# Kernel optimization log

Measured on AMD Instinct MI355X. Metric: run time of the kernel, lower is better.

Reference implementation:

```python
import jax, jax.numpy as jnp
import numpy as np

B, T, HID = 2, 2048, 1024
NH = 8
QK_DIM = 1024
V_DIM = 2048
SCALE_BASE = 512.0
GN_EPS = 1e-5


def _xpos_rotate(x, downscale):
    # x: [B, T, QK_DIM]; XPOS rotary embedding (syncdoth/RetNet, offset=0)
    d = QK_DIM
    dh = d // 2
    pos = jnp.arange(T, dtype=jnp.float32)
    # per-pair magnitude scale
    base_scale = (jnp.arange(0, d, 2, dtype=jnp.float32) + 0.4 * d) / (1.4 * d)  # [dh]
    scale = base_scale[None, :] ** (pos[:, None] / SCALE_BASE)  # [T, dh]
    if downscale:
        scale = 1.0 / scale
    inv_freq = 1.0 / (10000.0 ** (jnp.arange(dh, dtype=jnp.float32) / dh))
    sinusoid = pos[:, None] * inv_freq[None, :]  # [T, dh]
    sin = jnp.sin(sinusoid) * scale
    cos = jnp.cos(sinusoid) * scale
    # duplicate_interleave -> [T, d]
    sin = jnp.repeat(sin, 2, axis=-1)
    cos = jnp.repeat(cos, 2, axis=-1)
    x1 = x[..., 0::2]
    x2 = x[..., 1::2]
    rot = jnp.stack((-x2, x1), axis=-1).reshape(x.shape)  # rotate_every_two
    return x * cos[None] + rot * sin[None]


def setup_inputs() -> dict:
    key = jax.random.key(0)
    k1, k2, k3, k4 = jax.random.split(key, 4)
    x = jax.random.normal(k1, (B, T, HID), dtype=jnp.float32)
    Wqkv = jax.random.normal(k2, (HID, 2 * QK_DIM + V_DIM), dtype=jnp.float32) / np.sqrt(HID)
    Wg = jax.random.normal(k3, (HID, V_DIM), dtype=jnp.float32) / np.sqrt(HID)
    Wp = jax.random.normal(k4, (V_DIM, HID), dtype=jnp.float32) / np.sqrt(V_DIM)
    bp = jnp.zeros((HID,), dtype=jnp.float32)
    return {"x": x, "Wqkv": Wqkv, "Wg": Wg, "Wp": Wp, "bp": bp}


def reference(x, Wqkv, Wg, Wp, bp):
    # multi-scale decay (non-default gamma path)
    gamma = 1.0 - jnp.exp(jnp.linspace(np.log(1.0 / 32), np.log(1.0 / 512), NH)).astype(jnp.float32)  # [NH]

    qkv = x @ Wqkv  # [B,T,2qk+v]
    q, k, v = jnp.split(qkv, [QK_DIM, 2 * QK_DIM], axis=-1)
    q = _xpos_rotate(q, downscale=False)
    k = _xpos_rotate(k, downscale=True)

    dqk = QK_DIM // NH
    dv = V_DIM // NH
    q = q.reshape(B, T, NH, dqk).transpose(0, 2, 1, 3)  # [B,H,T,dqk]
    k = k.reshape(B, T, NH, dqk).transpose(0, 2, 1, 3)
    v = v.reshape(B, T, NH, dv).transpose(0, 2, 1, 3)   # [B,H,T,dv]

    # parallel decay mask: gamma^(i-j) for i>=j else 0  -> [H,T,T]
    idx = jnp.arange(T)
    expo = idx[:, None] - idx[None, :]
    expo_safe = jnp.where(expo >= 0, expo, 0).astype(jnp.float32)
    decay_mask = jnp.where(expo[None] >= 0, gamma[:, None, None] ** expo_safe[None], 0.0)  # [H,T,T]

    scores = jnp.einsum('bhid,bhjd->bhij', q, k) * (dqk ** -0.5)
    retention = jnp.einsum('bhij,bhjv->bhiv', scores * decay_mask[None], v)  # [B,H,T,dv]

    # current_kv state: sum_t decay_mask[h,-1,t] * k_t (outer) v_t  -> [B,H,dqk,dv]
    curr_kv = jnp.einsum('bhtk,bhtv,ht->bhkv', k, v, decay_mask[:, -1, :])

    ret = retention.transpose(0, 2, 1, 3).reshape(B, T, V_DIM)

    # GroupNorm(num_groups=NH, affine=False) over [B*T, V_DIM]
    g = ret.reshape(B, T, NH, dv)
    mu = jnp.mean(g, axis=-1, keepdims=True)
    var = jnp.var(g, axis=-1, keepdims=True)
    normed = ((g - mu) / jnp.sqrt(var + GN_EPS)).reshape(B, T, V_DIM)

    gate = jax.nn.silu(x @ Wg)
    out = (gate * normed) @ Wp + bp
    return out, curr_kv
```

## Files before the change

### kernel.cpp

```cpp
#include <hip/hip_runtime.h>

typedef unsigned short u16;
typedef unsigned int   u32;
typedef unsigned long long u64;

typedef __attribute__((ext_vector_type(8))) short bf8_t;
typedef __attribute__((ext_vector_type(4))) float f4_t;

#define DEVI __device__ __forceinline__
#define MFMA16(a,b,c) __builtin_amdgcn_mfma_f32_16x16x32_bf16((a),(b),(c),0,0,0)

#define BB   2
#define TT   2048
#define HIDN 1024
#define L0f  (-3.4657359027997265f)
#define DLf  (-0.3960841031714215f)
#define SCL  (0.08838834764831845f)

DEVI u16 f2b(float f) {
    u32 u = __float_as_uint(f);
    u += 0x7FFFu + ((u >> 16) & 1u);
    return (u16)(u >> 16);
}
DEVI float b2f(u16 u) { return __uint_as_float(((u32)u) << 16); }

DEVI void gll16(const void* g, void* l) {
    __builtin_amdgcn_global_load_lds((const __attribute__((address_space(1))) void*)g,
                                     (__attribute__((address_space(3))) void*)l, 16, 0, 0);
}

__global__ __launch_bounds__(256) void k_tables(u32* __restrict__ cqp, u32* __restrict__ ckp) {
    int idx = blockIdx.x * 256 + threadIdx.x;
    int t = idx >> 9, m = idx & 511;
    float base = (2.f * (float)m + 409.6f) * (1.f / 1433.6f);
    float s = exp2f(log2f(base) * ((float)t * (1.f / 512.f)));
    float invf = exp2f(-(float)m * (13.287712379549449f / 512.f));
    float sn, cs;
    sincosf((float)t * invf, &sn, &cs);
    int h = m >> 6;
    float lg2h = log2f(1.f - expf(L0f + (float)h * DLf));
    float qf = s * SCL * exp2f((float)(t & 63) * lg2h);
    cqp[idx] = (u32)f2b(cs * qf) | ((u32)f2b(sn * qf) << 16);
    float is = 1.f / s;
    ckp[idx] = (u32)f2b(cs * is) | ((u32)f2b(sn * is) << 16);
}

__global__ __launch_bounds__(256) void k_gpow(float* __restrict__ gt, float* __restrict__ gk) {
    if (blockIdx.x == 64) {
#pragma unroll
        for (int s = 0; s < 2; s++) {
            int idx = threadIdx.x + s * 256;
            int h = idx >> 6, d = idx & 63;
            float lg2 = log2f(1.f - expf(L0f + (float)h * DLf));
            gk[idx] = exp2f(-(float)d * lg2);
        }
        return;
    }
    int i = blockIdx.x * 256 + threadIdx.x;
    int h = i >> 11, t = i & 2047;
    float lg2 = log2f(1.f - expf(L0f + (float)h * DLf));
    gt[i] = exp2f((float)(2047 - t) * lg2);
}

__global__ __launch_bounds__(256) void k_cvt(const float* __restrict__ in, u16* __restrict__ out) {
    int i = blockIdx.x * 256 + threadIdx.x;
    float4 v = ((const float4*)in)[i];
    u64 pk = (u64)f2b(v.x) | ((u64)f2b(v.y) << 16) | ((u64)f2b(v.z) << 32) | ((u64)f2b(v.w) << 48);
    ((u64*)out)[i] = pk;
}

__global__ __launch_bounds__(256) void k_tpose(const float* __restrict__ in, u16* __restrict__ out,
                                               int R, int C) {
    __shared__ float tile[32][33];
    int c0 = blockIdx.x * 32, r0 = blockIdx.y * 32;
    int tx = threadIdx.x, ty = threadIdx.y;
#pragma unroll
    for (int i = 0; i < 4; i++)
        tile[ty * 4 + i][tx] = in[(size_t)(r0 + ty * 4 + i) * C + c0 + tx];
    __syncthreads();
#pragma unroll
    for (int i = 0; i < 4; i++)
        out[(size_t)(c0 + ty * 4 + i) * R + r0 + tx] = f2b(tile[tx][ty * 4 + i]);
}

DEVI void stage_tile(const u16* __restrict__ A, const u16* __restrict__ B,
                     int m0, int n0, int kt, char* buf, int tid, int wid) {
#pragma unroll
    for (int q = 0; q < 4; q++) {
        int flat = q * 8192 + tid * 16;
        int row = flat >> 7, byt = (flat & 127) ^ ((row & 7) << 4);
        gll16((const char*)A + (size_t)(m0 + row) * 2048 + kt * 128 + byt,
              buf + q * 8192 + wid * 1024);
        gll16((const char*)B + (size_t)(n0 + row) * 2048 + kt * 128 + byt,
              buf + 32768 + q * 8192 + wid * 1024);
    }
}

#define QPHASE(kk, fmh, LOADB)                                                        \
    {                                                                                 \
        bf8_t a_[4];                                                                  \
        _Pragma("unroll")                                                             \
        for (int f = 0; f < 4; f++) {                                                 \
            int ra = 128 * wr + ((fmh) * 4 + f) * 16 + lr;                            \
            a_[f] = *(const bf8_t*)(bA + ra * 128 + (((kk) * 64 + lg * 16) ^ ((ra & 7) << 4))); \
        }                                                                             \
        if (LOADB) {                                                                  \
            _Pragma("unroll")                                                         \
            for (int f = 0; f < 4; f++) {                                             \
                int rb = 64 * wc + f * 16 + lr;                                       \
                breg[f] = *(const bf8_t*)(bB + rb * 128 + (((kk) * 64 + lg * 16) ^ ((rb & 7) << 4))); \
            }                                                                         \
        }                                                                             \
        __builtin_amdgcn_s_barrier();                                                 \
        __builtin_amdgcn_s_setprio(1);                                                \
        _Pragma("unroll")                                                             \
        for (int f = 0; f < 4; f++)                                                   \
            _Pragma("unroll")                                                         \
            for (int j = 0; j < 4; j++)                                               \
                acc[(fmh) * 4 + f][j] = MFMA16(a_[f], breg[j], acc[(fmh) * 4 + f][j]); \
        __builtin_amdgcn_s_setprio(0);                                                \
        __builtin_amdgcn_s_barrier();                                                 \
    }

__global__ __launch_bounds__(512, 2) void k_gemm_qkvg8(
    const u16* __restrict__ xb, const u16* __restrict__ Wcat,
    const u32* __restrict__ cqp, const u32* __restrict__ ckp, const float* __restrict__ gkt,
    u16* __restrict__ qw, u16* __restrict__ kw, u16* __restrict__ kT, u16* __restrict__ vT,
    u16* __restrict__ gateb) {
    __shared__ __align__(16) char L[131072];
    int flat = blockIdx.x;
    int swz = (flat & 7) * 48 + (flat >> 3);
    int m0 = (swz / 24) * 256, n0 = (swz % 24) * 256;
    int tid = threadIdx.x, lane = tid & 63, wid = tid >> 6;
    int wr = wid >> 2, wc = wid & 3, lr = lane & 15, lg = lane >> 4;
    f4_t acc[8][4];
#pragma unroll
    for (int i = 0; i < 8; i++)
#pragma unroll
        for (int j = 0; j < 4; j++)
#pragma unroll
            for (int e = 0; e < 4; e++) acc[i][j][e] = 0.f;
    stage_tile(xb, Wcat, m0, n0, 0, L, tid, wid);
    __syncthreads();
    for (int kt = 0; kt < 16; ++kt) {
        const char* bA = L + (kt & 1) * 65536;
        const char* bB = bA + 32768;
        if (kt < 15) stage_tile(xb, Wcat, m0, n0, kt + 1, L + ((kt + 1) & 1) * 65536, tid, wid);
        bf8_t breg[4];
        QPHASE(0, 0, 1)
        QPHASE(0, 1, 0)
        QPHASE(1, 0, 1)
        QPHASE(1, 1, 0)
        __syncthreads();
    }
    char* SP = L;
    int b = m0 >> 11, t0 = m0 & 2047;
    if (n0 < 4096 && n0 >= 2048) {
        int h = (n0 - 2048) >> 8;
#pragma unroll
        for (int fm = 0; fm < 8; fm++)
#pragma unroll
            for (int fn = 0; fn < 4; fn++) {
                int dv = wc * 64 + fn * 16 + lr;
                int rowb = wr * 128 + fm * 16 + lg * 4;
                u64 pk = 0;
#pragma unroll
                for (int r = 0; r < 4; r++) pk |= ((u64)f2b(acc[fm][fn][r])) << (16 * r);
                *(u64*)(SP + dv * 512 + ((rowb * 2) ^ ((dv & 15) << 4))) = pk;
            }
        __syncthreads();
#pragma unroll
        for (int it = 0; it < 16; it++) {
            int chunk = it * 512 + tid;
            int dv = chunk >> 5, j = chunk & 31;
            uint4 v = *(const uint4*)(SP + dv * 512 + ((j * 16) ^ ((dv & 15) << 4)));
            *(uint4*)(vT + ((size_t)((b * 8 + h) * 256 + dv)) * 2048 + t0 + j * 8) = v;
        }
    } else if (n0 < 2048) {
        int isK = n0 >= 1024;
        const u32* cT = isK ? ckp : cqp;
        int hb = (n0 >> 7) & 7;
#pragma unroll
        for (int fm = 0; fm < 8; fm++)
#pragma unroll
            for (int fn = 0; fn < 4; fn++) {
                int col = wc * 64 + fn * 16 + lr;
                int gq = (n0 & 1023) + col;
                int mi = gq >> 1, h = gq >> 7;
                u64 pk = 0;
#pragma unroll
                for (int r = 0; r < 4; r++) {
                    int rowl = wr * 128 + fm * 16 + lg * 4 + r;
                    int t = t0 + rowl;
                    float v = acc[fm][fn][r];
                    float pv = __shfl_xor(v, 1);
                    u32 cp = cT[t * 512 + mi];
                    float cs = b2f((u16)cp), sn = b2f((u16)(cp >> 16));
                    float o = (col & 1) ? (v * cs + pv * sn) : (v * cs - pv * sn);
                    if (isK) {
                        pk |= ((u64)f2b(o)) << (16 * r);
                        o *= gkt[h * 64 + (t & 63)];
                    }
                    *(u16*)(SP + rowl * 512 + ((col * 2) ^ ((rowl & 15) << 4))) = f2b(o);
                }
                if (isK)
                    *(u64*)&kT[((size_t)((b * 8 + h) * 128 + (gq & 127))) * 2048 + t0 + wr * 128 + fm * 16 + lg * 4] = pk;
            }
        __syncthreads();
#pragma unroll
        for (int it = 0; it < 16; it++) {
            int chunk = it * 512 + tid;
            int r = chunk >> 5, j = chunk & 31;
            uint4 v = *(const uint4*)(SP + r * 512 + ((j * 16) ^ ((r & 15) << 4)));
            int hh = hb + (j >> 4);
            u16* g = (isK ? kw : qw) + ((size_t)((b * 8 + hh) * 2048 + t0 + r)) * 128 + (j & 15) * 8;
            *(uint4*)g = v;
        }
    } else {
        int c0 = n0 - 4096;
#pragma unroll
        for (int fm = 0; fm < 8; fm++)
#pragma unroll
            for (int fn = 0; fn < 4; fn++) {
                int col = wc * 64 + fn * 16 + lr;
#pragma unroll
                for (int r = 0; r < 4; r++) {
                    int rowl = wr * 128 + fm * 16 + lg * 4 + r;
                    float gg = acc[fm][fn][r];
                    *(u16*)(SP + rowl * 512 + ((col * 2) ^ ((rowl & 15) << 4))) = f2b(gg / (1.f + expf(-gg)));
                }
            }
        __syncthreads();
#pragma unroll
        for (int it = 0; it < 16; it++) {
            int chunk = it * 512 + tid;
            int r = chunk >> 5, j = chunk & 31;
            uint4 v = *(const uint4*)(SP + r * 512 + ((j * 16) ^ ((r & 15) << 4)));
            *(uint4*)(gateb + (size_t)(b * 2048 + t0 + r) * 2048 + c0 + j * 8) = v;
        }
    }
}

DEVI void gemm_ml(const u16* __restrict__ Ag, const u16* __restrict__ Bg, int Klen, int Kstr,
                  int m0, int n0, u16* As, u16* Bs, f4_t acc[4][4]) {
    int tid = threadIdx.x, lane = tid & 63, wid = tid >> 6;
    int wr = wid >> 1, wc = wid & 1, lr = lane & 15, lg = lane >> 4;
    for (int k0 = 0; k0 < Klen; k0 += 64) {
        __syncthreads();
#pragma unroll
        for (int p = 0; p < 4; p++) {
            int flat = p * 4096 + tid * 16;
            int row = flat >> 7, byt = (flat & 127) ^ ((row & 7) << 4);
            gll16((const char*)Ag + ((size_t)(m0 + row) * Kstr + k0) * 2 + byt,
                  (char*)As + p * 4096 + wid * 1024);
            gll16((const char*)Bg + ((size_t)(n0 + row) * Kstr + k0) * 2 + byt,
                  (char*)Bs + p * 4096 + wid * 1024);
        }
        __syncthreads();
#pragma unroll
        for (int kk = 0; kk < 2; kk++) {
            bf8_t a[4], b[4];
#pragma unroll
            for (int f = 0; f < 4; f++) {
                int ra = wr * 64 + f * 16 + lr;
                a[f] = *(const bf8_t*)((const char*)As + ra * 128 + ((kk * 64 + lg * 16) ^ ((ra & 7) << 4)));
                int rb = wc * 64 + f * 16 + lr;
                b[f] = *(const bf8_t*)((const char*)Bs + rb * 128 + ((kk * 64 + lg * 16) ^ ((rb & 7) << 4)));
            }
#pragma unroll
            for (int i = 0; i < 4; i++)
#pragma unroll
                for (int j = 0; j < 4; j++)
                    acc[i][j] = MFMA16(a[i], b[j], acc[i][j]);
        }
    }
}

DEVI void acc_zero(f4_t acc[4][4]) {
#pragma unroll
    for (int i = 0; i < 4; i++)
#pragma unroll
        for (int j = 0; j < 4; j++)
#pragma unroll
            for (int e = 0; e < 4; e++) acc[i][j][e] = 0.f;
}

__global__ __launch_bounds__(256) void k_gemm_outp(const u16* __restrict__ gdb, const u16* __restrict__ Wt,
                                                   float* __restrict__ part) {
    __shared__ u16 SM[128 * 128];
    f4_t acc[4][4]; acc_zero(acc);
    int m0 = blockIdx.y * 128, n0 = blockIdx.x * 128, kz = blockIdx.z;
    gemm_ml(gdb + kz * 1024, Wt + kz * 1024, 1024, 2048, m0, n0, SM, SM + 128 * 64, acc);
    int tid = threadIdx.x, lane = tid & 63, wid = tid >> 6;
    int wr = wid >> 1, wc = wid & 1, lr = lane & 15, lg = lane >> 4;
    float* SMf = (float*)SM;
    float* po = part + (size_t)kz * 4096 * 1024;
    __syncthreads();
#pragma unroll
    for (int p = 0; p < 2; p++) {
        if (p) __syncthreads();
        if (wr == p) {
#pragma unroll
            for (int fm = 0; fm < 4; fm++)
#pragma unroll
                for (int fn = 0; fn < 4; fn++) {
                    int col = wc * 64 + fn * 16 + lr;
#pragma unroll
                    for (int r = 0; r < 4; r++) {
                        int rowl = fm * 16 + lg * 4 + r;
                        *(float*)((char*)SMf + rowl * 512 + ((col * 4) ^ ((rowl & 7) << 6))) = acc[fm][fn][r];
                    }
                }
        }
        __syncthreads();
#pragma unroll
        for (int it2 = 0; it2 < 8; it2++) {
            int chunk = it2 * 256 + tid;
            int rowl = chunk >> 5, j = chunk & 31;
            f4_t v = *(const f4_t*)((const char*)SMf + rowl * 512 + ((j * 16) ^ ((rowl & 7) << 6)));
            *(f4_t*)((char*)po + ((size_t)(m0 + p * 64 + rowl) * 1024 + n0) * 4 + j * 16) = v;
        }
    }
}

__global__ __launch_bounds__(256) void k_outred(const float* __restrict__ part, const float* __restrict__ bp,
                                                float* __restrict__ outp) {
    int i = blockIdx.x * 256 + threadIdx.x;
    f4_t a = ((const f4_t*)part)[i];
    f4_t c = ((const f4_t*)(part + (size_t)4096 * 1024))[i];
    f4_t bb = *(const f4_t*)(bp + ((i * 4) & 1023));
#pragma unroll
    for (int e = 0; e < 4; e++) a[e] += c[e] + bb[e];
    ((f4_t*)outp)[i] = a;
}

__global__ __launch_bounds__(256, 3) void k_retention(const u16* __restrict__ qws, const u16* __restrict__ kws,
                                                      const u16* __restrict__ vTws,
                                                      u16* __restrict__ ret0, u16* __restrict__ ret1) {
    __shared__ u16 SMr[64 * 128 + 256 * 64];
    u16* Ks = SMr;
    u16* Vs = SMr + 64 * 128;
    int x = blockIdx.x;
    int it, jlo, jhi, toret1;
    if (x < 16)      { it = 15 - x;  jlo = 0;              jhi = it + 1;         toret1 = 0; }
    else if (x < 32) { it = x;       jlo = 0;              jhi = (it + 2) >> 1;  toret1 = 0; }
    else             { it = x - 16;  jlo = (it + 2) >> 1;  jhi = it + 1;         toret1 = 1; }
    int h = blockIdx.y, b = blockIdx.z;
    int bh = b * 8 + h;
    float lg2 = log2f(1.f - expf(L0f + (float)h * DLf));
    int i0 = it * 64;
    const u16* qbase = qws + (size_t)bh * 2048 * 128;
    const u16* kbase = kws + (size_t)bh * 2048 * 128;
    const u16* vbase = vTws + (size_t)bh * 256 * 2048;
    int tid = threadIdx.x, lane = tid & 63, w = tid >> 6, lr = lane & 15, lg = lane >> 4;
    bf8_t aq[4];
#pragma unroll
    for (int kk = 0; kk < 4; kk++)
        aq[kk] = *(const bf8_t*)((const char*)qbase + (size_t)(i0 + w * 16 + lr) * 256 + kk * 64 + lg * 16);
    f4_t racc[16];
#pragma unroll
    for (int f = 0; f < 16; f++)
#pragma unroll
        for (int e = 0; e < 4; e++) racc[f][e] = 0.f;
    for (int jt = jlo; jt < jhi; jt++) {
        int j0 = jt * 64;
        int diag = (jt == it);
        float tf = exp2f(64.f * (float)(it - jt) * lg2);
        __syncthreads();
#pragma unroll
        for (int p = 0; p < 4; p++) {
            int flat = p * 4096 + tid * 16;
            int row = flat >> 8, byt = (flat & 255) ^ ((row & 7) << 4);
            gll16((const char*)kbase + (size_t)(j0 + row) * 256 + byt, (char*)Ks + p * 4096 + w * 1024);
        }
#pragma unroll
        for (int p = 0; p < 8; p++) {
            int flat = p * 4096 + tid * 16;
            int row = flat >> 7, byt = (flat & 127) ^ ((row & 7) << 4);
            gll16((const char*)vbase + (size_t)row * 4096 + (size_t)j0 * 2 + byt,
                  (char*)Vs + p * 4096 + w * 1024);
        }
        __syncthreads();
        f4_t sacc[4];
#pragma unroll
        for (int f = 0; f < 4; f++)
#pragma unroll
            for (int e = 0; e < 4; e++) sacc[f][e] = 0.f;
#pragma unroll
        for (int kk = 0; kk < 4; kk++)
#pragma unroll
            for (int fn = 0; fn < 4; fn++) {
                int rb = fn * 16 + lr;
                bf8_t bb = *(const bf8_t*)((const char*)Ks + rb * 256 + ((kk * 64 + lg * 16) ^ ((rb & 7) << 4)));
                sacc[fn] = MFMA16(aq[kk], bb, sacc[fn]);
            }
        __syncthreads();
#pragma unroll
        for (int fn = 0; fn < 4; fn++)
#pragma unroll
            for (int r = 0; r < 4; r++) {
                int i_loc = w * 16 + lg * 4 + r;
                int col = fn * 16 + lr;
                float v = diag ? ((i_loc - col >= 0) ? sacc[fn][r] : 0.f) : sacc[fn][r] * tf;
                *(u16*)((char*)Ks + i_loc * 128 + ((col * 2) ^ ((i_loc & 7) << 4))) = f2b(v);
            }
#pragma unroll
        for (int kk = 0; kk < 2; kk++) {
            int ra = w * 16 + lr;
            bf8_t ap = *(const bf8_t*)((const char*)Ks + ra * 128 + ((kk * 64 + lg * 16) ^ ((ra & 7) << 4)));
#pragma unroll
            for (int fn2 = 0; fn2 < 16; fn2++) {
                int rb = fn2 * 16 + lr;
                bf8_t bv = *(const bf8_t*)((const char*)Vs + rb * 128 + ((kk * 64 + lg * 16) ^ ((rb & 7) << 4)));
                racc[fn2] = MFMA16(ap, bv, racc[fn2]);
            }
        }
    }
    __syncthreads();
    u16* St = Vs;
#pragma unroll
    for (int fn2 = 0; fn2 < 16; fn2++)
#pragma unroll
        for (int r = 0; r < 4; r++) {
            int il = w * 16 + lg * 4 + r;
            int dv = fn2 * 16 + lr;
            *(u16*)((char*)St + il * 512 + ((dv * 2) ^ ((il & 15) << 4))) = f2b(racc[fn2][r]);
        }
    __syncthreads();
#pragma unroll
    for (int it2 = 0; it2 < 8; it2++) {
        int chunk = it2 * 256 + tid;
        int il = chunk >> 5, j = chunk & 31;
        uint4 v = *(const uint4*)((const char*)St + il * 512 + ((j * 16) ^ ((il & 15) << 4)));
        char* dst;
        if (toret1) dst = (char*)ret1 + ((size_t)(b * 1024 + i0 - 1024 + il) * 2048 + h * 256) * 2 + j * 16;
        else        dst = (char*)ret0 + ((size_t)(b * 2048 + i0 + il) * 2048 + h * 256) * 2 + j * 16;
        *(uint4*)dst = v;
    }
}

__global__ __launch_bounds__(512) void k_currkv(const u16* __restrict__ kTws, const u16* __restrict__ vTws,
                                                const float* __restrict__ gtab, float* __restrict__ part) {
    __shared__ u16 Ks2[128 * 64];
    __shared__ u16 Vws[256 * 64];
    int tr = blockIdx.x;
    int bh = blockIdx.y;
    int h = bh & 7;
    const u16* kT = kTws + (size_t)bh * 128 * 2048;
    const u16* vT = vTws + (size_t)bh * 256 * 2048;
    const float* gt = gtab + h * 2048;
    int tid = threadIdx.x, lane = tid & 63, wid = tid >> 6;
    int wr = wid >> 2, wc = wid & 3, lr = lane & 15, lg = lane >> 4;
    f4_t acc[4][4]; acc_zero(acc);
    for (int tc = 0; tc < 8; tc++) {
        int t0 = tr * 512 + tc * 64;
        __syncthreads();
#pragma unroll
        for (int p = 0; p < 2; p++) {
            int flat = p * 8192 + tid * 16;
            int row = flat >> 7, byt = (flat & 127) ^ ((row & 7) << 4);
            gll16((const char*)kT + (size_t)row * 4096 + (size_t)t0 * 2 + byt,
                  (char*)Ks2 + p * 8192 + wid * 1024);
        }
#pragma unroll
        for (int p = 0; p < 4; p++) {
            int flat = p * 8192 + tid * 16;
            int row = flat >> 7, byt = flat & 127;
            int tt = t0 + (byt >> 1);
            const u16* src = vT + (size_t)row * 2048 + tt;
            u16 tmp[8]; *(uint4*)tmp = *(const uint4*)src;
            const float* gp = gt + tt;
            u16 op[8];
#pragma unroll
            for (int e = 0; e < 8; e++) op[e] = f2b(b2f(tmp[e]) * gp[e]);
            *(uint4*)((char*)Vws + row * 128 + (byt ^ ((row & 7) << 4))) = *(uint4*)op;
        }
        __syncthreads();
#pragma unroll
        for (int kk = 0; kk < 2; kk++) {
            bf8_t a[4], bb[4];
#pragma unroll
            for (int f = 0; f < 4; f++) {
                int ra = wr * 64 + f * 16 + lr;
                a[f] = *(const bf8_t*)((const char*)Ks2 + ra * 128 + ((kk * 64 + lg * 16) ^ ((ra & 7) << 4)));
                int rb = wc * 64 + f * 16 + lr;
                bb[f] = *(const bf8_t*)((const char*)Vws + rb * 128 + ((kk * 64 + lg * 16) ^ ((rb & 7) << 4)));
            }
#pragma unroll
            for (int i = 0; i < 4; i++)
#pragma unroll
                for (int j = 0; j < 4; j++)
                    acc[i][j] = MFMA16(a[i], bb[j], acc[i][j]);
        }
    }
#pragma unroll
    for (int fm = 0; fm < 4; fm++)
#pragma unroll
        for (int fn = 0; fn < 4; fn++)
#pragma unroll
            for (int r = 0; r < 4; r++) {
                int dk = wr * 64 + fm * 16 + lg * 4 + r;
                int dv = wc * 64 + fn * 16 + lr;
                part[((size_t)(bh * 4 + tr)) * 32768 + (size_t)dk * 256 + dv] = acc[fm][fn][r];
            }
}

__global__ __launch_bounds__(256) void k_reduce_ckv(const float* __restrict__ part, float* __restrict__ outc) {
    int i = blockIdx.x * 256 + threadIdx.x;
    int bh = i >> 15, wv = i & 32767;
    float s = 0.f;
#pragma unroll
    for (int tr = 0; tr < 4; tr++) s += part[((size_t)(bh * 4 + tr)) * 32768 + wv];
    outc[i] = s;
}

__global__ __launch_bounds__(256) void k_gnorm(const u16* __restrict__ ret0, const u16* __restrict__ ret1,
                                               const u16* __restrict__ gateb, u16* __restrict__ gatedb) {
    int g = blockIdx.x * 4 + (threadIdx.x >> 6);
    int lane = threadIdx.x & 63;
    int row = g >> 3, h = g & 7;
    size_t base = (size_t)row * 2048 + h * 256 + lane * 4;
    u64 p0 = *(const u64*)(ret0 + base);
    float e0 = b2f((u16)p0), e1 = b2f((u16)(p0 >> 16)), e2 = b2f((u16)(p0 >> 32)), e3 = b2f((u16)(p0 >> 48));
    if ((row & 2047) >= 1024) {
        size_t b1 = (size_t)((row >> 11) * 1024 + (row & 1023)) * 2048 + h * 256 + lane * 4;
        u64 p1 = *(const u64*)(ret1 + b1);
        e0 += b2f((u16)p1); e1 += b2f((u16)(p1 >> 16)); e2 += b2f((u16)(p1 >> 32)); e3 += b2f((u16)(p1 >> 48));
    }
    float s = e0 + e1 + e2 + e3;
    float sqs = e0 * e0 + e1 * e1 + e2 * e2 + e3 * e3;
#pragma unroll
    for (int m = 1; m < 64; m <<= 1) { s += __shfl_xor(s, m); sqs += __shfl_xor(sqs, m); }
    float mean = s * (1.f / 256.f);
    float var = sqs * (1.f / 256.f) - mean * mean;
    float inv = rsqrtf(var + 1e-5f);
    u64 gp = *(const u64*)(gateb + base);
    u64 pk = (u64)f2b((e0 - mean) * inv * b2f((u16)gp)) |
             ((u64)f2b((e1 - mean) * inv * b2f((u16)(gp >> 16))) << 16) |
             ((u64)f2b((e2 - mean) * inv * b2f((u16)(gp >> 32))) << 32) |
             ((u64)f2b((e3 - mean) * inv * b2f((u16)(gp >> 48))) << 48);
    *(u64*)(gatedb + base) = pk;
}

extern "C" void kernel_launch(void* const* d_in, const int* in_sizes, int n_in,
                              void* d_out, int out_size, void* d_ws, size_t ws_size,
                              hipStream_t stream) {
    const float* x    = (const float*)d_in[0];
    const float* Wqkv = (const float*)d_in[1];
    const float* Wg   = (const float*)d_in[2];
    const float* Wp   = (const float*)d_in[3];
    const float* bp   = (const float*)d_in[4];
    float* outp   = (float*)d_out;
    float* outckv = outp + (size_t)BB * TT * HIDN;

    char* ws = (char*)d_ws;
    const size_t MB = 1024 * 1024;
    u16*   xb     = (u16*)(ws);
    u16*   WqkvT  = (u16*)(ws + 8 * MB);
    u16*   WgT    = (u16*)(ws + 16 * MB);
    u16*   WpT    = (u16*)(ws + 20 * MB);
    u32*   cqp    = (u32*)(ws + 24 * MB);
    u32*   ckp    = (u32*)(ws + 28 * MB);
    u16*   gateb  = (u16*)(ws + 32 * MB);
    u16*   qw     = (u16*)(ws + 48 * MB);
    u16*   kw     = (u16*)(ws + 56 * MB);
    u16*   kT     = (u16*)(ws + 64 * MB);
    u16*   vT     = (u16*)(ws + 72 * MB);
    u16*   ret0b  = (u16*)(ws + 88 * MB);
    u16*   ret1b  = (u16*)(ws + 104 * MB);
    float* ckvp   = (float*)(ws + 112 * MB);
    float* gtab   = (float*)(ws + 120 * MB);
    float* gkt    = (float*)(ws + 120 * MB + 65536);
    u16*   gatedb = (u16*)(ws + 48 * MB);
    float* opart  = (float*)(ws + 88 * MB);

    hipLaunchKernelGGL(k_tables, dim3(4096), dim3(256), 0, stream, cqp, ckp);
    hipLaunchKernelGGL(k_gpow, dim3(65), dim3(256), 0, stream, gtab, gkt);
    hipLaunchKernelGGL(k_cvt, dim3(4096), dim3(256), 0, stream, x, xb);
    hipLaunchKernelGGL(k_tpose, dim3(128, 32), dim3(32, 8), 0, stream, Wqkv, WqkvT, 1024, 4096);
    hipLaunchKernelGGL(k_tpose, dim3(64, 32),  dim3(32, 8), 0, stream, Wg,   WgT,   1024, 2048);
    hipLaunchKernelGGL(k_tpose, dim3(32, 64),  dim3(32, 8), 0, stream, Wp,   WpT,   2048, 1024);
    hipLaunchKernelGGL(k_gemm_qkvg8, dim3(384), dim3(512), 0, stream,
                       xb, WqkvT, cqp, ckp, gkt, qw, kw, kT, vT, gateb);
    hipLaunchKernelGGL(k_currkv, dim3(4, 16), dim3(512), 0, stream, kT, vT, gtab, ckvp);
    hipLaunchKernelGGL(k_reduce_ckv, dim3(2048), dim3(256), 0, stream, ckvp, outckv);
    hipLaunchKernelGGL(k_retention, dim3(48, 8, 2), dim3(256), 0, stream, qw, kw, vT, ret0b, ret1b);
    hipLaunchKernelGGL(k_gnorm, dim3(8192), dim3(256), 0, stream, ret0b, ret1b, gateb, gatedb);
    hipLaunchKernelGGL(k_gemm_outp, dim3(8, 32, 2), dim3(256), 0, stream, gatedb, WpT, opart);
    hipLaunchKernelGGL(k_outred, dim3(4096), dim3(256), 0, stream, opart, bp, outp);
}
```

Baseline: 231.3 us.

## Double-buffer out-projection GEMM and relax barriers with partial vmcnt waits

The output-projection GEMM moves from a single-buffered load-then-compute loop to a double-buffered LDS pipeline. The next K-tile is prefetched while the current one is consumed, and the code waits with a partial vmcnt count instead of draining all loads. The QKV/gate GEMM gets the same fine-grained wait-plus-s_barrier scheme in place of a full __syncthreads, and its block-to-tile mapping changes so that M varies fastest within N column groups. This is meant to hide global load latency and reduce barrier stalls. In exchange it doubles LDS use in the out-proj kernel and relies on hand-counted vmcnt values staying correct.

```diff
diff --git a/kernel.cpp b/kernel.cpp
--- a/kernel.cpp
+++ b/kernel.cpp
@@ -130,7 +130,8 @@
     __shared__ __align__(16) char L[131072];
     int flat = blockIdx.x;
     int swz = (flat & 7) * 48 + (flat >> 3);
-    int m0 = (swz / 24) * 256, n0 = (swz % 24) * 256;
+    int n0 = (swz >> 4) * 256;
+    int m0 = (swz & 15) * 256;
     int tid = threadIdx.x, lane = tid & 63, wid = tid >> 6;
     int wr = wid >> 2, wc = wid & 3, lr = lane & 15, lg = lane >> 4;
     f4_t acc[8][4];
@@ -141,17 +142,23 @@
 #pragma unroll
             for (int e = 0; e < 4; e++) acc[i][j][e] = 0.f;
     stage_tile(xb, Wcat, m0, n0, 0, L, tid, wid);
-    __syncthreads();
+    asm volatile("s_waitcnt vmcnt(0)" ::: "memory");
+    __builtin_amdgcn_s_barrier();
     for (int kt = 0; kt < 16; ++kt) {
         const char* bA = L + (kt & 1) * 65536;
         const char* bB = bA + 32768;
-        if (kt < 15) stage_tile(xb, Wcat, m0, n0, kt + 1, L + ((kt + 1) & 1) * 65536, tid, wid);
+        if (kt < 15) {
+            stage_tile(xb, Wcat, m0, n0, kt + 1, L + ((kt + 1) & 1) * 65536, tid, wid);
+            asm volatile("s_waitcnt vmcnt(8)" ::: "memory");
+        } else {
+            asm volatile("s_waitcnt vmcnt(0)" ::: "memory");
+        }
+        __builtin_amdgcn_s_barrier();
         bf8_t breg[4];
         QPHASE(0, 0, 1)
         QPHASE(0, 1, 0)
         QPHASE(1, 0, 1)
         QPHASE(1, 1, 0)
-        __syncthreads();
     }
     char* SP = L;
     int b = m0 >> 11, t0 = m0 & 2047;
@@ -241,31 +248,59 @@
     }
 }
 
-DEVI void gemm_ml(const u16* __restrict__ Ag, const u16* __restrict__ Bg, int Klen, int Kstr,
-                  int m0, int n0, u16* As, u16* Bs, f4_t acc[4][4]) {
+DEVI void acc_zero(f4_t acc[4][4]) {
+#pragma unroll
+    for (int i = 0; i < 4; i++)
+#pragma unroll
+        for (int j = 0; j < 4; j++)
+#pragma unroll
+            for (int e = 0; e < 4; e++) acc[i][j][e] = 0.f;
+}
+
+DEVI void stage128(const u16* __restrict__ A, const u16* __restrict__ B, int Kstr,
+                   int m0, int n0, int kt, char* buf, int tid, int wid) {
+#pragma unroll
+    for (int p = 0; p < 4; p++) {
+        int flat = p * 4096 + tid * 16;
+        int row = flat >> 7, byt = (flat & 127) ^ ((row & 7) << 4);
+        gll16((const char*)A + ((size_t)(m0 + row) * Kstr + kt * 64) * 2 + byt,
+              buf + p * 4096 + wid * 1024);
+        gll16((const char*)B + ((size_t)(n0 + row) * Kstr + kt * 64) * 2 + byt,
+              buf + 16384 + p * 4096 + wid * 1024);
+    }
+}
+
+__global__ __launch_bounds__(256) void k_gemm_outp(const u16* __restrict__ gdb, const u16* __restrict__ Wt,
+                                                   float* __restrict__ part) {
+    __shared__ __align__(16) char Lo[65536];
+    int m0 = blockIdx.y * 128, n0 = blockIdx.x * 128, kz = blockIdx.z;
+    const u16* Ag = gdb + kz * 1024;
+    const u16* Bg = Wt + kz * 1024;
     int tid = threadIdx.x, lane = tid & 63, wid = tid >> 6;
     int wr = wid >> 1, wc = wid & 1, lr = lane & 15, lg = lane >> 4;
-    for (int k0 = 0; k0 < Klen; k0 += 64) {
-        __syncthreads();
-#pragma unroll
-        for (int p = 0; p < 4; p++) {
-            int flat = p * 4096 + tid * 16;
-            int row = flat >> 7, byt = (flat & 127) ^ ((row & 7) << 4);
-            gll16((const char*)Ag + ((size_t)(m0 + row) * Kstr + k0) * 2 + byt,
-                  (char*)As + p * 4096 + wid * 1024);
-            gll16((const char*)Bg + ((size_t)(n0 + row) * Kstr + k0) * 2 + byt,
-                  (char*)Bs + p * 4096 + wid * 1024);
-        }
-        __syncthreads();
+    f4_t acc[4][4]; acc_zero(acc);
+    stage128(Ag, Bg, 2048, m0, n0, 0, Lo, tid, wid);
+    asm volatile("s_waitcnt vmcnt(0)" ::: "memory");
+    __builtin_amdgcn_s_barrier();
+    for (int kt = 0; kt < 16; ++kt) {
+        const char* bA = Lo + (kt & 1) * 32768;
+        const char* bB = bA + 16384;
+        if (kt < 15) {
+            stage128(Ag, Bg, 2048, m0, n0, kt + 1, Lo + ((kt + 1) & 1) * 32768, tid, wid);
+            asm volatile("s_waitcnt vmcnt(8)" ::: "memory");
+        } else {
+            asm volatile("s_waitcnt vmcnt(0)" ::: "memory");
+        }
+        __builtin_amdgcn_s_barrier();
 #pragma unroll
         for (int kk = 0; kk < 2; kk++) {
             bf8_t a[4], b[4];
 #pragma unroll
             for (int f = 0; f < 4; f++) {
                 int ra = wr * 64 + f * 16 + lr;
-                a[f] = *(const bf8_t*)((const char*)As + ra * 128 + ((kk * 64 + lg * 16) ^ ((ra & 7) << 4)));
+                a[f] = *(const bf8_t*)(bA + ra * 128 + ((kk * 64 + lg * 16) ^ ((ra & 7) << 4)));
                 int rb = wc * 64 + f * 16 + lr;
-                b[f] = *(const bf8_t*)((const char*)Bs + rb * 128 + ((kk * 64 + lg * 16) ^ ((rb & 7) << 4)));
+                b[f] = *(const bf8_t*)(bB + rb * 128 + ((kk * 64 + lg * 16) ^ ((rb & 7) << 4)));
             }
 #pragma unroll
             for (int i = 0; i < 4; i++)
@@ -273,27 +308,9 @@
                 for (int j = 0; j < 4; j++)
                     acc[i][j] = MFMA16(a[i], b[j], acc[i][j]);
         }
-    }
-}
-
-DEVI void acc_zero(f4_t acc[4][4]) {
-#pragma unroll
-    for (int i = 0; i < 4; i++)
-#pragma unroll
-        for (int j = 0; j < 4; j++)
-#pragma unroll
-            for (int e = 0; e < 4; e++) acc[i][j][e] = 0.f;
-}
-
-__global__ __launch_bounds__(256) void k_gemm_outp(const u16* __restrict__ gdb, const u16* __restrict__ Wt,
-                                                   float* __restrict__ part) {
-    __shared__ u16 SM[128 * 128];
-    f4_t acc[4][4]; acc_zero(acc);
-    int m0 = blockIdx.y * 128, n0 = blockIdx.x * 128, kz = blockIdx.z;
-    gemm_ml(gdb + kz * 1024, Wt + kz * 1024, 1024, 2048, m0, n0, SM, SM + 128 * 64, acc);
-    int tid = threadIdx.x, lane = tid & 63, wid = tid >> 6;
-    int wr = wid >> 1, wc = wid & 1, lr = lane & 15, lg = lane >> 4;
-    float* SMf = (float*)SM;
+        __builtin_amdgcn_s_barrier();
+    }
+    float* SMf = (float*)Lo;
     float* po = part + (size_t)kz * 4096 * 1024;
     __syncthreads();
 #pragma unroll
```

Result: slower. 272.8 us (+18.0%).
